# Kernel optimization log

Measured on AMD Instinct MI355X. Metric: run time of the kernel, lower is better.

## Reference

```python
import jax, jax.numpy as jnp
import numpy as np

HEAD = 128
E = 1536
MAXPOS = 2048

def _rope_tables(seq_len, d):
    # get_sinusoid_encoding_table: col 2i = sin(pos/10000^(2i/d)), col 2i+1 = cos(same)
    pos = np.arange(seq_len, dtype=np.float32)[:, None]
    i = np.arange(d // 2, dtype=np.float32)
    ang = pos / np.power(10000.0, 2.0 * i / d)  # [seq, d/2]
    cos_pos = np.repeat(np.cos(ang), 2, axis=-1)  # table[:,1::2] repeat_interleave(2)
    sin_pos = np.repeat(np.sin(ang), 2, axis=-1)  # table[:,0::2] repeat_interleave(2)
    return jnp.asarray(cos_pos), jnp.asarray(sin_pos)

def _apply_rope(x, cos_pos, sin_pos):
    # x: [b, s, d]; rotate pairs (x0,x1) -> (-x1, x0)
    x2 = jnp.stack([-x[..., 1::2], x[..., ::2]], axis=-1).reshape(x.shape)
    return x * cos_pos + x2 * sin_pos

def setup_inputs() -> dict:
    key = jax.random.key(0)
    ks = jax.random.split(key, 6)
    b, s, h = 4, 2048, 768
    return {
        "hidden_states": jax.random.normal(ks[0], (b, s, h), jnp.float32),
        "attention_mask": jnp.ones((b, 1, 1, s), jnp.float32),
        "Wi": jax.random.normal(ks[1], (h, 2 * E + HEAD), jnp.float32) * 0.02,
        "bi": jnp.zeros((2 * E + HEAD,), jnp.float32),
        "gamma": 1.0 + jax.random.normal(ks[2], (2, HEAD), jnp.float32) * 0.02,
        "beta": jnp.zeros((2, HEAD), jnp.float32),
        "Wo": jax.random.normal(ks[3], (E, h), jnp.float32) * 0.02,
        "bo": jnp.zeros((h,), jnp.float32),
    }

def reference(hidden_states, attention_mask, Wi, bi, gamma, beta, Wo, bo):
    b, s, _ = hidden_states.shape
    x = jax.nn.silu(hidden_states @ Wi + bi)  # hidden_act='swish'
    u, v, qk = jnp.split(x, [E, 2 * E], axis=-1)  # [b,s,E],[b,s,E],[b,s,HEAD]
    # OffsetScale with 2 heads -> q, k
    q = qk * gamma[0] + beta[0]
    k = qk * gamma[1] + beta[1]
    cos_pos, sin_pos = _rope_tables(s, HEAD)
    q = _apply_rope(q, cos_pos, sin_pos)
    k = _apply_rope(k, cos_pos, sin_pos)
    scores = jnp.einsum('bid,bjd->bij', q, k) / jnp.sqrt(jnp.float32(HEAD))
    add_mask = (1.0 - attention_mask) * -1e12  # [b,1,1,s]
    scores = scores + jnp.squeeze(add_mask, axis=1)  # broadcast [b,1,s]
    # softmax_plus normalization
    valid = (scores > -1e11).astype(scores.dtype)
    l = jnp.maximum(jnp.sum(valid, axis=-1, keepdims=True), 1.0)
    scale = jnp.log(l) / jnp.log(jnp.float32(512.0))
    attn = jax.nn.softmax(scores * scale, axis=-1)
    out = (u * jnp.einsum('bij,bjd->bid', attn, v)) @ Wo + bo
    return out
```

## Files before the change

### kernel.cpp

```cpp
#include <hip/hip_runtime.h>
#include <math.h>

typedef _Float16 f16;
typedef _Float16 f16x8 __attribute__((ext_vector_type(8)));
typedef float f32x4 __attribute__((ext_vector_type(4)));

#define HEAD 128
#define EDIM 1536
#define NI   3200
#define NIP  3328
#define HDIM 768
#define BATCH 4
#define SEQ  2048
#define MTOT (BATCH*SEQ)

__device__ __forceinline__ void gld_lds16(const void* g, void* l) {
  __builtin_amdgcn_global_load_lds(
      (const __attribute__((address_space(1))) void*)g,
      (__attribute__((address_space(3))) void*)l, 16, 0, 0);
}

__global__ __launch_bounds__(256) void cast_f32_f16_k(const float* __restrict__ in,
                                                      f16* __restrict__ out, int n4) {
  int i = blockIdx.x * 256 + threadIdx.x;
  if (i >= n4) return;
  float4 x = ((const float4*)in)[i];
  union { f16 h[4]; short4 s; } u;
  u.h[0] = (f16)x.x; u.h[1] = (f16)x.y; u.h[2] = (f16)x.z; u.h[3] = (f16)x.w;
  ((short4*)out)[i] = u.s;
}

__global__ __launch_bounds__(256) void transpose_cast_k(const float* __restrict__ in, int ld_in,
                                                        f16* __restrict__ out, int ld_out) {
  __shared__ float tile[32][33];
  int c = threadIdx.x & 31, r0 = threadIdx.x >> 5;
  int ib = blockIdx.y * 32, jb = blockIdx.x * 32;
#pragma unroll
  for (int rr = 0; rr < 32; rr += 8)
    tile[r0 + rr][c] = in[(size_t)(ib + r0 + rr) * ld_in + jb + c];
  __syncthreads();
#pragma unroll
  for (int rr = 0; rr < 32; rr += 8)
    out[(size_t)(jb + r0 + rr) * ld_out + ib + c] = (f16)tile[c][r0 + rr];
}

__global__ __launch_bounds__(256) void transpose_f16_k(const f16* __restrict__ in, int ld_in,
                                                       long long sIn,
                                                       f16* __restrict__ out, int ld_out,
                                                       long long sOut) {
  __shared__ f16 tile[32][33];
  in  += (size_t)blockIdx.z * sIn;
  out += (size_t)blockIdx.z * sOut;
  int c = threadIdx.x & 31, r0 = threadIdx.x >> 5;
  int ib = blockIdx.y * 32, jb = blockIdx.x * 32;
#pragma unroll
  for (int rr = 0; rr < 32; rr += 8)
    tile[r0 + rr][c] = in[(size_t)(ib + r0 + rr) * ld_in + jb + c];
  __syncthreads();
#pragma unroll
  for (int rr = 0; rr < 32; rr += 8)
    out[(size_t)(jb + r0 + rr) * ld_out + ib + c] = tile[c][r0 + rr];
}

__global__ __launch_bounds__(256) void rope_tables_k(float* __restrict__ cosT,
                                                     float* __restrict__ sinT) {
  int id = blockIdx.x * 256 + threadIdx.x;
  int pos = id >> 6, i = id & 63;
  float ang = (float)pos / powf(10000.0f, (float)(2 * i) / 128.0f);
  float cv = cosf(ang), sv = sinf(ang);
  cosT[pos * HEAD + 2 * i]     = cv;
  cosT[pos * HEAD + 2 * i + 1] = cv;
  sinT[pos * HEAD + 2 * i]     = sv;
  sinT[pos * HEAD + 2 * i + 1] = sv;
}

__global__ __launch_bounds__(256) void addmask_k(const float* __restrict__ mask,
                                                 float* __restrict__ am) {
  int i = blockIdx.x * 256 + threadIdx.x;
  am[i] = (1.0f - mask[i]) * -1e12f;
}

__global__ __launch_bounds__(256) void rope_gate_k(const f16* __restrict__ qkraw,
                                                   const float* __restrict__ gamma,
                                                   const float* __restrict__ beta,
                                                   const float* __restrict__ cosT,
                                                   const float* __restrict__ sinT,
                                                   f16* __restrict__ Qh,
                                                   f16* __restrict__ Kh) {
  int id = blockIdx.x * 256 + threadIdx.x;
  int row = id >> 4, c0i = (id & 15) * 8;
  int pos = row & (SEQ - 1);
  f16x8 sv8 = *(const f16x8*)(qkraw + (size_t)row * HEAD + c0i);
  f16 oq[8], ok[8];
#pragma unroll
  for (int e = 0; e < 8; e += 2) {
    int c = c0i + e;
    float cs = cosT[pos * HEAD + c], sn = sinT[pos * HEAD + c];
    float s0 = (float)sv8[e], s1 = (float)sv8[e + 1];
    float q0 = s0 * gamma[c] + beta[c];
    float q1 = s1 * gamma[c + 1] + beta[c + 1];
    oq[e]     = (f16)(q0 * cs - q1 * sn);
    oq[e + 1] = (f16)(q1 * cs + q0 * sn);
    float k0 = s0 * gamma[128 + c] + beta[128 + c];
    float k1 = s1 * gamma[128 + c + 1] + beta[128 + c + 1];
    ok[e]     = (f16)(k0 * cs - k1 * sn);
    ok[e + 1] = (f16)(k1 * cs + k0 * sn);
  }
  *(f16x8*)(Qh + (size_t)row * HEAD + c0i) = *(f16x8*)oq;
  *(f16x8*)(Kh + (size_t)row * HEAD + c0i) = *(f16x8*)ok;
}

template <int MODE>
__global__ __launch_bounds__(512, 2)
void gemm8p(const f16* __restrict__ A, int lda,
            const f16* __restrict__ B0, int ldb, long long sB, int bshift, int K,
            f16* __restrict__ outH, f16* __restrict__ outH2,
            const float* __restrict__ c0, const f16* __restrict__ hA) {
  __shared__ f16 LS[2][2][2][2][4096];
  int bx, by;
  {
    int gx = gridDim.x;
    int id = blockIdx.y * gx + blockIdx.x;
    int cpx = (gx * gridDim.y) >> 3;
    int sw = (id & 7) * cpx + (id >> 3);
    bx = sw % gx; by = sw / gx;
  }
  const int m0 = by * 256, n0 = bx * 256;
  const int t = threadIdx.x;
  const int lane = t & 63, w = t >> 6;
  const int wr = w >> 2, wc = w & 3;
  const int lr = lane & 15, kg = lane >> 4;
  const int bb = by >> bshift;
  const f16* Bb = B0 + (size_t)bb * sB;

  const int rb = t >> 3;
  const int sl = ((t & 7) ^ (rb & 7)) << 3;
  const f16* gA = A  + (size_t)(m0 + rb) * lda + sl;
  const f16* gB = Bb + (size_t)(n0 + rb) * ldb + sl;
  char* lA = (char*)LS + w * 1024;
  char* lB = (char*)LS + 32768 + w * 1024;

  auto stageA = [&](int kt, int h) {
    const f16* s = gA + (size_t)(h << 7) * lda + (kt << 6);
    char* d = lA + ((kt & 1) << 16) + (h << 14);
    gld_lds16(s, d);
    gld_lds16(s + ((size_t)lda << 6), d + 8192);
  };
  auto stageB = [&](int kt, int h) {
    const f16* s = gB + (size_t)(h << 7) * ldb + (kt << 6);
    char* d = lB + ((kt & 1) << 16) + (h << 14);
    gld_lds16(s, d);
    gld_lds16(s + ((size_t)ldb << 6), d + 8192);
  };

  const char* RA = (const char*)LS + ((wr * 128 + lr) << 7);
  const char* RB = (const char*)LS + 32768 + ((wc * 64 + lr) << 7);
  const int sw0 = (kg ^ (lr & 7)) << 4;
  const int sw1 = ((4 + kg) ^ (lr & 7)) << 4;

  f32x4 acc[8][4];
#pragma unroll
  for (int i = 0; i < 8; ++i)
#pragma unroll
    for (int j = 0; j < 4; ++j) acc[i][j] = f32x4{0.f, 0.f, 0.f, 0.f};

  const int nt = K >> 6;
  stageA(0, 0); stageA(0, 1); stageB(0, 0); stageB(0, 1);
  asm volatile("" ::: "memory");
  if (nt > 1) {
    stageB(1, 0); stageB(1, 1);
    asm volatile("s_waitcnt vmcnt(4)" ::: "memory");
  } else {
    asm volatile("s_waitcnt vmcnt(0)" ::: "memory");
  }
  __builtin_amdgcn_s_barrier();
  asm volatile("" ::: "memory");

  for (int tt = 0; tt < nt; ++tt) {
    const char* SA = RA + ((tt & 1) << 16);
    const char* SB = RB + ((tt & 1) << 16);
    f16x8 a0[4][2], a1[4][2], b0[2][2], b1[2][2];
#pragma unroll
    for (int i2 = 0; i2 < 4; ++i2) {
      a0[i2][0] = *(const f16x8*)(SA + (i2 << 11) + sw0);
      a0[i2][1] = *(const f16x8*)(SA + (i2 << 11) + sw1);
    }
#pragma unroll
    for (int j2 = 0; j2 < 2; ++j2) {
      b0[j2][0] = *(const f16x8*)(SB + (j2 << 11) + sw0);
      b0[j2][1] = *(const f16x8*)(SB + (j2 << 11) + sw1);
    }
    if (tt + 1 < nt) stageA(tt + 1, 0);
    __builtin_amdgcn_s_barrier();
    asm volatile("" ::: "memory");
    __builtin_amdgcn_s_setprio(1);
#pragma unroll
    for (int ks = 0; ks < 2; ++ks)
#pragma unroll
      for (int i2 = 0; i2 < 4; ++i2)
#pragma unroll
        for (int j2 = 0; j2 < 2; ++j2)
          acc[i2][j2] = __builtin_amdgcn_mfma_f32_16x16x32_f16(
              a0[i2][ks], b0[j2][ks], acc[i2][j2], 0, 0, 0);
    __builtin_amdgcn_s_setprio(0);
    __builtin_amdgcn_s_barrier();
    asm volatile("" ::: "memory");
#pragma unroll
    for (int j2 = 0; j2 < 2; ++j2) {
      b1[j2][0] = *(const f16x8*)(SB + ((2 + j2) << 11) + sw0);
      b1[j2][1] = *(const f16x8*)(SB + ((2 + j2) << 11) + sw1);
    }
    if (tt + 1 < nt) stageA(tt + 1, 1);
    __builtin_amdgcn_s_barrier();
    asm volatile("" ::: "memory");
    __builtin_amdgcn_s_setprio(1);
#pragma unroll
    for (int ks = 0; ks < 2; ++ks)
#pragma unroll
      for (int i2 = 0; i2 < 4; ++i2)
#pragma unroll
        for (int j2 = 0; j2 < 2; ++j2)
          acc[i2][2 + j2] = __builtin_amdgcn_mfma_f32_16x16x32_f16(
              a0[i2][ks], b1[j2][ks], acc[i2][2 + j2], 0, 0, 0);
    __builtin_amdgcn_s_setprio(0);
    __builtin_amdgcn_s_barrier();
    asm volatile("" ::: "memory");
#pragma unroll
    for (int i2 = 0; i2 < 4; ++i2) {
      a1[i2][0] = *(const f16x8*)(SA + ((4 + i2) << 11) + sw0);
      a1[i2][1] = *(const f16x8*)(SA + ((4 + i2) << 11) + sw1);
    }
    if (tt + 2 < nt) stageB(tt + 2, 0);
    __builtin_amdgcn_s_barrier();
    asm volatile("" ::: "memory");
    __builtin_amdgcn_s_setprio(1);
#pragma unroll
    for (int ks = 0; ks < 2; ++ks)
#pragma unroll
      for (int i2 = 0; i2 < 4; ++i2)
#pragma unroll
        for (int j2 = 0; j2 < 2; ++j2)
          acc[4 + i2][j2] = __builtin_amdgcn_mfma_f32_16x16x32_f16(
              a1[i2][ks], b0[j2][ks], acc[4 + i2][j2], 0, 0, 0);
    __builtin_amdgcn_s_setprio(0);
    __builtin_amdgcn_s_barrier();
    asm volatile("" ::: "memory");
    if (tt + 2 < nt) stageB(tt + 2, 1);
    __builtin_amdgcn_s_barrier();
    asm volatile("" ::: "memory");
    __builtin_amdgcn_s_setprio(1);
#pragma unroll
    for (int ks = 0; ks < 2; ++ks)
#pragma unroll
      for (int i2 = 0; i2 < 4; ++i2)
#pragma unroll
        for (int j2 = 0; j2 < 2; ++j2)
          acc[4 + i2][2 + j2] = __builtin_amdgcn_mfma_f32_16x16x32_f16(
              a1[i2][ks], b1[j2][ks], acc[4 + i2][2 + j2], 0, 0, 0);
    __builtin_amdgcn_s_setprio(0);
    if (tt + 2 < nt) asm volatile("s_waitcnt vmcnt(4)" ::: "memory");
    else             asm volatile("s_waitcnt vmcnt(0)" ::: "memory");
    __builtin_amdgcn_s_barrier();
    asm volatile("" ::: "memory");
  }

  if (MODE == 2) {
    const int colbase = n0 + wc * 64;
#pragma unroll
    for (int i = 0; i < 8; ++i)
#pragma unroll
      for (int j = 0; j < 4; ++j)
#pragma unroll
        for (int r = 0; r < 4; ++r) {
          int row = m0 + wr * 128 + i * 16 + kg * 4 + r;
          int col = colbase + j * 16 + lr;
          float uu = (float)hA[(size_t)row * 3072 + col];
          outH[(size_t)row * EDIM + col] = (f16)(acc[i][j][r] * uu);
        }
    return;
  }
  if (MODE == 1 && bx == 12) {
    const int colbase = n0 + wc * 64;
    if (colbase >= 3200) return;
#pragma unroll
    for (int i = 0; i < 8; ++i)
#pragma unroll
      for (int j = 0; j < 4; ++j)
#pragma unroll
        for (int r = 0; r < 4; ++r) {
          int row = m0 + wr * 128 + i * 16 + kg * 4 + r;
          int col = colbase + j * 16 + lr;
          float xb = acc[i][j][r] + c0[col];
          float s = xb * __builtin_amdgcn_rcpf(1.0f + __expf(-xb));
          outH2[row * HEAD + (col - 3072)] = (f16)s;
        }
    return;
  }
  f16* OT = (f16*)LS;
#pragma unroll
  for (int i = 0; i < 8; ++i) {
#pragma unroll
    for (int j = 0; j < 4; ++j) {
#pragma unroll
      for (int r = 0; r < 4; ++r) {
        int row = wr * 128 + i * 16 + kg * 4 + r;
        int col = wc * 64 + j * 16 + lr;
        float xb = acc[i][j][r] + c0[n0 + col];
        f16 v = (f16)(xb * __builtin_amdgcn_rcpf(1.0f + __expf(-xb)));
        OT[row * 256 + ((((col >> 3) ^ (row & 7)) << 3) | (col & 7))] = v;
      }
    }
  }
  __syncthreads();
  const int tr = t >> 3, tc = t & 7;
#pragma unroll
  for (int rp = 0; rp < 4; ++rp) {
#pragma unroll
    for (int cc = 0; cc < 4; ++cc) {
      int row = rp * 64 + tr;
      int cIdx = cc * 8 + tc;
      f16x8 vv = *(const f16x8*)&OT[row * 256 + ((cIdx ^ (row & 7)) << 3)];
      *(f16x8*)&outH[(size_t)(m0 + row) * 3072 + n0 + cIdx * 8] = vv;
    }
  }
}

__global__ __launch_bounds__(256, 2)
void scores_os(const f16* __restrict__ Q, const f16* __restrict__ Kt,
               f16* __restrict__ P, const float* __restrict__ am) {
  __shared__ f16 Qs[128 * 128];
  __shared__ f16 Ks[128 * 128];
  const int z = blockIdx.z;
  const int m0 = blockIdx.y * 128, n0 = blockIdx.x * 128;
  const int t = threadIdx.x;
  const int lane = t & 63, w = t >> 6;
  const int wr = w >> 1, wc = w & 1;
  const int lr = lane & 15, kg = lane >> 4;

  const f16* Qb = Q  + (size_t)z * SEQ * HEAD;
  const f16* Kb = Kt + (size_t)z * SEQ * HEAD;

  const int rq = t >> 4, l = t & 15;
#pragma unroll
  for (int c = 0; c < 8; ++c) {
    int row = c * 16 + rq;
    int lq = l ^ (row & 15);
    gld_lds16(Qb + (size_t)(m0 + row) * HEAD + lq * 8, (char*)Qs + c * 4096 + w * 1024);
    gld_lds16(Kb + (size_t)(n0 + row) * HEAD + lq * 8, (char*)Ks + c * 4096 + w * 1024);
  }
  asm volatile("s_waitcnt vmcnt(0)" ::: "memory");
  __syncthreads();

  f32x4 acc[4][4];
#pragma unroll
  for (int i = 0; i < 4; ++i)
#pragma unroll
    for (int j = 0; j < 4; ++j) acc[i][j] = f32x4{0.f, 0.f, 0.f, 0.f};

#pragma unroll
  for (int kk = 0; kk < 4; ++kk) {
    f16x8 af[4], bf[4];
#pragma unroll
    for (int i = 0; i < 4; ++i) {
      int rA = wr * 64 + i * 16 + lr;
      af[i] = *(const f16x8*)&Qs[rA * 128 + (((kk * 4 + kg) ^ (rA & 15)) << 3)];
      int rB = wc * 64 + i * 16 + lr;
      bf[i] = *(const f16x8*)&Ks[rB * 128 + (((kk * 4 + kg) ^ (rB & 15)) << 3)];
    }
#pragma unroll
    for (int i = 0; i < 4; ++i)
#pragma unroll
      for (int j = 0; j < 4; ++j)
        acc[i][j] = __builtin_amdgcn_mfma_f32_16x16x32_f16(af[i], bf[j], acc[i][j], 0, 0, 0);
  }

  f16* outP = P + (size_t)z * SEQ * SEQ;
  const float* c = am + (size_t)z * SEQ;
#pragma unroll
  for (int i = 0; i < 4; ++i)
#pragma unroll
    for (int j = 0; j < 4; ++j)
#pragma unroll
      for (int r = 0; r < 4; ++r) {
        int row = m0 + wr * 64 + i * 16 + kg * 4 + r;
        int col = n0 + wc * 64 + j * 16 + lr;
        outP[(size_t)row * SEQ + col] = (f16)(acc[i][j][r] * 0.08838834764831845f + c[col]);
      }
}

__global__ __launch_bounds__(256, 4)
void gemm_final(const f16* __restrict__ A, int lda,
                const f16* __restrict__ Bt, int ldb, int K,
                float* __restrict__ outF, const float* __restrict__ c0) {
  __shared__ f16 As0[128 * 32], As1[128 * 32], Bs0[128 * 32], Bs1[128 * 32];
  int bx, by;
  {
    int gx = gridDim.x;
    int id = blockIdx.y * gx + blockIdx.x;
    int cpx = (gx * gridDim.y) >> 3;
    int sw = (id & 7) * cpx + (id >> 3);
    bx = sw % gx; by = sw / gx;
  }
  const int m0 = by * 128, n0 = bx * 128;
  const int t = threadIdx.x;
  const int lane = t & 63, w = t >> 6;
  const int wr = w >> 1, wc = w & 1;
  const int lr = lane & 15, kg = lane >> 4;

  const f16* ga = A  + (size_t)(m0 + (t >> 2)) * lda + (t & 3) * 8;
  const f16* gb = Bt + (size_t)(n0 + (t >> 2)) * ldb + (t & 3) * 8;

  f32x4 acc[4][4];
#pragma unroll
  for (int i = 0; i < 4; ++i)
#pragma unroll
    for (int j = 0; j < 4; ++j) acc[i][j] = f32x4{0.f, 0.f, 0.f, 0.f};

  auto stage = [&](f16* AS, f16* BS, int kk) {
    gld_lds16(ga + kk,                    (char*)AS + w * 1024);
    gld_lds16(ga + (size_t)64 * lda + kk, (char*)AS + w * 1024 + 4096);
    gld_lds16(gb + kk,                    (char*)BS + w * 1024);
    gld_lds16(gb + (size_t)64 * ldb + kk, (char*)BS + w * 1024 + 4096);
  };
  auto compute = [&](const f16* AS, const f16* BS) {
    f16x8 af[4], bf[4];
#pragma unroll
    for (int i = 0; i < 4; ++i) {
      af[i] = *(const f16x8*)&AS[(wr * 64 + i * 16 + lr) * 32 + kg * 8];
      bf[i] = *(const f16x8*)&BS[(wc * 64 + i * 16 + lr) * 32 + kg * 8];
    }
#pragma unroll
    for (int i = 0; i < 4; ++i)
#pragma unroll
      for (int j = 0; j < 4; ++j)
        acc[i][j] = __builtin_amdgcn_mfma_f32_16x16x32_f16(af[i], bf[j], acc[i][j], 0, 0, 0);
  };

  stage(As0, Bs0, 0);
  __syncthreads();
  for (int k0 = 0; k0 < K; k0 += 64) {
    if (k0 + 32 < K) stage(As1, Bs1, k0 + 32);
    compute(As0, Bs0);
    __syncthreads();
    if (k0 + 64 < K) stage(As0, Bs0, k0 + 64);
    compute(As1, Bs1);
    __syncthreads();
  }

#pragma unroll
  for (int i = 0; i < 4; ++i)
#pragma unroll
    for (int j = 0; j < 4; ++j)
#pragma unroll
      for (int r = 0; r < 4; ++r) {
        int row = m0 + wr * 64 + i * 16 + kg * 4 + r;
        int col = n0 + wc * 64 + j * 16 + lr;
        outF[(size_t)row * HDIM + col] = acc[i][j][r] + c0[col];
      }
}

__global__ __launch_bounds__(256) void softmax_plus_f16(f16* __restrict__ P) {
  __shared__ float red[4];
  const int t = threadIdx.x;
  f16* pr = P + (size_t)blockIdx.x * SEQ;
  union { uint4 u4; f16 h[8]; } ld;
  ld.u4 = ((const uint4*)pr)[t];
  float v[8];
#pragma unroll
  for (int i = 0; i < 8; ++i) v[i] = fmaxf((float)ld.h[i], -1e12f);

  float cnt = 0.f;
#pragma unroll
  for (int i = 0; i < 8; ++i) cnt += (v[i] > -1e11f) ? 1.0f : 0.0f;
#pragma unroll
  for (int o = 32; o; o >>= 1) cnt += __shfl_xor(cnt, o, 64);
  if ((t & 63) == 0) red[t >> 6] = cnt;
  __syncthreads();
  cnt = red[0] + red[1] + red[2] + red[3];
  float scale = __logf(fmaxf(cnt, 1.0f)) * 0.16025848f;

  float mx = -INFINITY;
#pragma unroll
  for (int i = 0; i < 8; ++i) { v[i] *= scale; mx = fmaxf(mx, v[i]); }
#pragma unroll
  for (int o = 32; o; o >>= 1) mx = fmaxf(mx, __shfl_xor(mx, o, 64));
  __syncthreads();
  if ((t & 63) == 0) red[t >> 6] = mx;
  __syncthreads();
  mx = fmaxf(fmaxf(red[0], red[1]), fmaxf(red[2], red[3]));

  float p[8], sum = 0.f;
#pragma unroll
  for (int i = 0; i < 8; ++i) { p[i] = __expf(v[i] - mx); sum += p[i]; }
#pragma unroll
  for (int o = 32; o; o >>= 1) sum += __shfl_xor(sum, o, 64);
  __syncthreads();
  if ((t & 63) == 0) red[t >> 6] = sum;
  __syncthreads();
  sum = red[0] + red[1] + red[2] + red[3];
  float inv = __builtin_amdgcn_rcpf(sum);

  union { f16 h[8]; uint4 u4; } pk;
#pragma unroll
  for (int i = 0; i < 8; ++i) pk.h[i] = (f16)(p[i] * inv);
  ((uint4*)pr)[t] = pk.u4;
}

extern "C" void kernel_launch(void* const* d_in, const int* in_sizes, int n_in,
                              void* d_out, int out_size, void* d_ws, size_t ws_size,
                              hipStream_t stream) {
  const float* hs    = (const float*)d_in[0];
  const float* mask  = (const float*)d_in[1];
  const float* Wi    = (const float*)d_in[2];
  const float* bi    = (const float*)d_in[3];
  const float* gamma = (const float*)d_in[4];
  const float* beta  = (const float*)d_in[5];
  const float* Wo    = (const float*)d_in[6];
  const float* bo    = (const float*)d_in[7];
  float* out = (float*)d_out;

  const int nb = (ws_size >= ((size_t)175 << 20)) ? BATCH : 1;

  char* p = (char*)d_ws;
  auto alloc = [&](size_t b) { char* r = p; p += (b + 255) & ~(size_t)255; return r; };
  f16*   Xh    = (f16*)  alloc((size_t)MTOT * 3072 * 2);
  f16*   qkraw = (f16*)  alloc((size_t)MTOT * HEAD * 2);
  f16*   Qh    = (f16*)  alloc((size_t)MTOT * HEAD * 2);
  f16*   Kh    = (f16*)  alloc((size_t)MTOT * HEAD * 2);
  f16*   Ah    = (f16*)  alloc((size_t)MTOT * HDIM * 2);
  f16*   WiT   = (f16*)  alloc((size_t)NIP * HDIM * 2);
  f16*   WoT   = (f16*)  alloc((size_t)HDIM * EDIM * 2);
  float* cosT  = (float*)alloc((size_t)SEQ * HEAD * 4);
  float* sinT  = (float*)alloc((size_t)SEQ * HEAD * 4);
  float* am    = (float*)alloc((size_t)BATCH * SEQ * 4);
  f16*   G     = (f16*)  alloc((size_t)MTOT * EDIM * 2);
  f16*   P     = (f16*)  alloc((size_t)nb * SEQ * SEQ * 2);
  f16*   Vt    = (f16*)  alloc((size_t)nb * EDIM * SEQ * 2);

  cast_f32_f16_k<<<dim3(MTOT * HDIM / 4 / 256), 256, 0, stream>>>(hs, Ah, MTOT * HDIM / 4);
  transpose_cast_k<<<dim3(NI / 32, HDIM / 32), 256, 0, stream>>>(Wi, NI, WiT, HDIM);
  transpose_cast_k<<<dim3(HDIM / 32, EDIM / 32), 256, 0, stream>>>(Wo, HDIM, WoT, EDIM);
  rope_tables_k<<<dim3(SEQ * 64 / 256), 256, 0, stream>>>(cosT, sinT);
  addmask_k<<<dim3(BATCH * SEQ / 256), 256, 0, stream>>>(mask, am);

  gemm8p<1><<<dim3(NIP / 256, MTOT / 256), 512, 0, stream>>>(
      Ah, HDIM, WiT, HDIM, 0, 30, HDIM,
      Xh, qkraw, bi, nullptr);
  rope_gate_k<<<dim3(MTOT * 16 / 256), 256, 0, stream>>>(
      qkraw, gamma, beta, cosT, sinT, Qh, Kh);

  const int bsh = (nb == BATCH) ? 3 : 30;
  for (int b0 = 0; b0 < BATCH; b0 += nb) {
    transpose_f16_k<<<dim3(EDIM / 32, SEQ / 32, nb), 256, 0, stream>>>(
        Xh + (size_t)b0 * SEQ * 3072 + 1536, 3072, (long long)SEQ * 3072,
        Vt, SEQ, (long long)EDIM * SEQ);
    scores_os<<<dim3(SEQ / 128, SEQ / 128, nb), 256, 0, stream>>>(
        Qh + (size_t)b0 * SEQ * HEAD, Kh + (size_t)b0 * SEQ * HEAD,
        P, am + b0 * SEQ);
    softmax_plus_f16<<<dim3(nb * SEQ), 256, 0, stream>>>(P);
    gemm8p<2><<<dim3(EDIM / 256, nb * SEQ / 256), 512, 0, stream>>>(
        P, SEQ, Vt, SEQ, (long long)EDIM * SEQ, bsh, SEQ,
        G + (size_t)b0 * SEQ * EDIM, nullptr, nullptr,
        Xh + (size_t)b0 * SEQ * 3072);
  }

  gemm_final<<<dim3(HDIM / 128, MTOT / 128), 256, 0, stream>>>(
      G, EDIM, WoT, EDIM, EDIM, out, bo);
}
```

Before: 214.6 us.

## Fuse V transpose into first GEMM epilogue, drop separate transpose kernel

New measurement: 204.7 us, median of 2. 1.05x faster.

```diff
diff --git a/kernel.cpp b/kernel.cpp
--- a/kernel.cpp
+++ b/kernel.cpp
@@ -42,24 +42,6 @@
 #pragma unroll
   for (int rr = 0; rr < 32; rr += 8)
     out[(size_t)(jb + r0 + rr) * ld_out + ib + c] = (f16)tile[c][r0 + rr];
-}
-
-__global__ __launch_bounds__(256) void transpose_f16_k(const f16* __restrict__ in, int ld_in,
-                                                       long long sIn,
-                                                       f16* __restrict__ out, int ld_out,
-                                                       long long sOut) {
-  __shared__ f16 tile[32][33];
-  in  += (size_t)blockIdx.z * sIn;
-  out += (size_t)blockIdx.z * sOut;
-  int c = threadIdx.x & 31, r0 = threadIdx.x >> 5;
-  int ib = blockIdx.y * 32, jb = blockIdx.x * 32;
-#pragma unroll
-  for (int rr = 0; rr < 32; rr += 8)
-    tile[r0 + rr][c] = in[(size_t)(ib + r0 + rr) * ld_in + jb + c];
-  __syncthreads();
-#pragma unroll
-  for (int rr = 0; rr < 32; rr += 8)
-    out[(size_t)(jb + r0 + rr) * ld_out + ib + c] = tile[c][r0 + rr];
 }
 
 __global__ __launch_bounds__(256) void rope_tables_k(float* __restrict__ cosT,
@@ -115,6 +97,7 @@
 void gemm8p(const f16* __restrict__ A, int lda,
             const f16* __restrict__ B0, int ldb, long long sB, int bshift, int K,
             f16* __restrict__ outH, f16* __restrict__ outH2,
+            f16* __restrict__ outV,
             const float* __restrict__ c0, const f16* __restrict__ hA) {
   __shared__ f16 LS[2][2][2][2][4096];
   int bx, by;
@@ -274,7 +257,7 @@
         for (int r = 0; r < 4; ++r) {
           int row = m0 + wr * 128 + i * 16 + kg * 4 + r;
           int col = colbase + j * 16 + lr;
-          float uu = (float)hA[(size_t)row * 3072 + col];
+          float uu = (float)hA[(size_t)row * EDIM + col];
           outH[(size_t)row * EDIM + col] = (f16)(acc[i][j][r] * uu);
         }
     return;
@@ -307,20 +290,43 @@
         int col = wc * 64 + j * 16 + lr;
         float xb = acc[i][j][r] + c0[n0 + col];
         f16 v = (f16)(xb * __builtin_amdgcn_rcpf(1.0f + __expf(-xb)));
-        OT[row * 256 + ((((col >> 3) ^ (row & 7)) << 3) | (col & 7))] = v;
+        int slot = ((col >> 3) ^ (row & 7) ^ ((row >> 3) & 7));
+        OT[row * 256 + ((slot << 3) | (col & 7))] = v;
       }
     }
   }
   __syncthreads();
-  const int tr = t >> 3, tc = t & 7;
-#pragma unroll
-  for (int rp = 0; rp < 4; ++rp) {
-#pragma unroll
-    for (int cc = 0; cc < 4; ++cc) {
-      int row = rp * 64 + tr;
-      int cIdx = cc * 8 + tc;
-      f16x8 vv = *(const f16x8*)&OT[row * 256 + ((cIdx ^ (row & 7)) << 3)];
-      *(f16x8*)&outH[(size_t)(m0 + row) * 3072 + n0 + cIdx * 8] = vv;
+  if (bx < 6) {
+    const int tr = t >> 3, tc = t & 7;
+#pragma unroll
+    for (int rp = 0; rp < 4; ++rp) {
+#pragma unroll
+      for (int cc = 0; cc < 4; ++cc) {
+        int row = rp * 64 + tr;
+        int cIdx = cc * 8 + tc;
+        int slot = (cIdx ^ (row & 7) ^ ((row >> 3) & 7));
+        f16x8 vv = *(const f16x8*)&OT[row * 256 + (slot << 3)];
+        *(f16x8*)&outH[(size_t)(m0 + row) * EDIM + n0 + cIdx * 8] = vv;
+      }
+    }
+  } else {
+    f16* Vtb = outV + (size_t)(by >> 3) * EDIM * SEQ;
+    const int vbase = n0 - EDIM;
+    const int rib0 = m0 & (SEQ - 1);
+    const int rg = t & 31;
+    const int cw = t >> 5;
+    const int fm = ((cw & 1) << 2) | ((cw >> 1) & 3) | ((cw >> 3) << 3);
+#pragma unroll
+    for (int it = 0; it < 16; ++it) {
+      int c = it * 16 + fm;
+      f16 seg[8];
+#pragma unroll
+      for (int e = 0; e < 8; ++e) {
+        int row = rg * 8 + e;
+        int slot = ((c >> 3) ^ (row & 7) ^ ((row >> 3) & 7));
+        seg[e] = OT[row * 256 + ((slot << 3) | (c & 7))];
+      }
+      *(f16x8*)&Vtb[(size_t)(vbase + c) * SEQ + rib0 + rg * 8] = *(f16x8*)seg;
     }
   }
 }
@@ -519,11 +525,12 @@
   const float* bo    = (const float*)d_in[7];
   float* out = (float*)d_out;
 
-  const int nb = (ws_size >= ((size_t)175 << 20)) ? BATCH : 1;
+  const int nb = (ws_size >= ((size_t)160 << 20)) ? BATCH : 1;
 
   char* p = (char*)d_ws;
   auto alloc = [&](size_t b) { char* r = p; p += (b + 255) & ~(size_t)255; return r; };
-  f16*   Xh    = (f16*)  alloc((size_t)MTOT * 3072 * 2);
+  f16*   Xh    = (f16*)  alloc((size_t)MTOT * EDIM * 2);
+  f16*   Vt    = (f16*)  alloc((size_t)BATCH * EDIM * SEQ * 2);
   f16*   qkraw = (f16*)  alloc((size_t)MTOT * HEAD * 2);
   f16*   Qh    = (f16*)  alloc((size_t)MTOT * HEAD * 2);
   f16*   Kh    = (f16*)  alloc((size_t)MTOT * HEAD * 2);
@@ -535,7 +542,6 @@
   float* am    = (float*)alloc((size_t)BATCH * SEQ * 4);
   f16*   G     = (f16*)  alloc((size_t)MTOT * EDIM * 2);
   f16*   P     = (f16*)  alloc((size_t)nb * SEQ * SEQ * 2);
-  f16*   Vt    = (f16*)  alloc((size_t)nb * EDIM * SEQ * 2);
 
   cast_f32_f16_k<<<dim3(MTOT * HDIM / 4 / 256), 256, 0, stream>>>(hs, Ah, MTOT * HDIM / 4);
   transpose_cast_k<<<dim3(NI / 32, HDIM / 32), 256, 0, stream>>>(Wi, NI, WiT, HDIM);
@@ -545,23 +551,20 @@
 
   gemm8p<1><<<dim3(NIP / 256, MTOT / 256), 512, 0, stream>>>(
       Ah, HDIM, WiT, HDIM, 0, 30, HDIM,
-      Xh, qkraw, bi, nullptr);
+      Xh, qkraw, Vt, bi, nullptr);
   rope_gate_k<<<dim3(MTOT * 16 / 256), 256, 0, stream>>>(
       qkraw, gamma, beta, cosT, sinT, Qh, Kh);
 
   const int bsh = (nb == BATCH) ? 3 : 30;
   for (int b0 = 0; b0 < BATCH; b0 += nb) {
-    transpose_f16_k<<<dim3(EDIM / 32, SEQ / 32, nb), 256, 0, stream>>>(
-        Xh + (size_t)b0 * SEQ * 3072 + 1536, 3072, (long long)SEQ * 3072,
-        Vt, SEQ, (long long)EDIM * SEQ);
     scores_os<<<dim3(SEQ / 128, SEQ / 128, nb), 256, 0, stream>>>(
         Qh + (size_t)b0 * SEQ * HEAD, Kh + (size_t)b0 * SEQ * HEAD,
         P, am + b0 * SEQ);
     softmax_plus_f16<<<dim3(nb * SEQ), 256, 0, stream>>>(P);
     gemm8p<2><<<dim3(EDIM / 256, nb * SEQ / 256), 512, 0, stream>>>(
-        P, SEQ, Vt, SEQ, (long long)EDIM * SEQ, bsh, SEQ,
-        G + (size_t)b0 * SEQ * EDIM, nullptr, nullptr,
-        Xh + (size_t)b0 * SEQ * 3072);
+        P, SEQ, Vt + (size_t)b0 * EDIM * SEQ, SEQ, (long long)EDIM * SEQ, bsh, SEQ,
+        G + (size_t)b0 * SEQ * EDIM, nullptr, nullptr, nullptr,
+        Xh + (size_t)b0 * SEQ * EDIM);
   }
 
   gemm_final<<<dim3(HDIM / 128, MTOT / 128), 256, 0, stream>>>(
```
